# Optimization experiments

Measured on AMD Instinct MI355X. Metric: run time of the kernel, lower is better.

## Reference

```python
import jax, jax.numpy as jnp
import numpy as np
import math

B, S, H, Dh, Dr, HID, C = 2, 2048, 16, 128, 64, 2048, 512

def _linear(x, w, b):
    return x @ w.T + b

def _rope(x):
    # x: [B, H, S, Dr]; interleaved-pair rotation as in the torch module
    d = x.shape[-1]
    s = x.shape[2]
    inv_freq = 1.0 / (10000.0 ** (jnp.arange(0, d, 2, dtype=jnp.float32) / d))
    sinusoid = jnp.arange(s, dtype=jnp.float32)[:, None] * inv_freq[None, :]  # [S, d/2]
    sin, cos = jnp.sin(sinusoid), jnp.cos(sinusoid)  # broadcast over B,H
    x1 = x[..., 0::2]
    x2 = x[..., 1::2]
    rot = jnp.stack([x1 * cos - x2 * sin, x1 * sin + x2 * cos], axis=-1)
    return rot.reshape(x.shape)

def setup_inputs() -> dict:
    key = jax.random.key(0)
    ks = jax.random.split(key, 9)
    sc = 0.02
    return {
        "x": jax.random.normal(ks[0], (B, S, HID), jnp.float32),
        "d_kv_w": jax.random.normal(ks[1], (C, HID), jnp.float32) * sc,
        "d_kv_b": jnp.zeros((C,), jnp.float32),
        "u_k_w": jax.random.normal(ks[2], (H * Dh, C), jnp.float32) * sc,
        "u_k_b": jnp.zeros((H * Dh,), jnp.float32),
        "u_v_w": jax.random.normal(ks[3], (H * Dh, C), jnp.float32) * sc,
        "u_v_b": jnp.zeros((H * Dh,), jnp.float32),
        "d_q_w": jax.random.normal(ks[4], (C, HID), jnp.float32) * sc,
        "d_q_b": jnp.zeros((C,), jnp.float32),
        "u_q_w": jax.random.normal(ks[5], (H * Dh, C), jnp.float32) * sc,
        "u_q_b": jnp.zeros((H * Dh,), jnp.float32),
        "qr_w": jax.random.normal(ks[6], (H * Dr, C), jnp.float32) * sc,
        "qr_b": jnp.zeros((H * Dr,), jnp.float32),
        "out_w": jax.random.normal(ks[7], (HID, H * Dh), jnp.float32) * sc,
        "out_b": jnp.zeros((HID,), jnp.float32),
    }

def reference(x, d_kv_w, d_kv_b, u_k_w, u_k_b, u_v_w, u_v_b,
              d_q_w, d_q_b, u_q_w, u_q_b, qr_w, qr_b, out_w, out_b):
    b, s, _ = x.shape
    kv_c = _linear(x, d_kv_w, d_kv_b)                      # [B,S,C]
    k_c = _linear(kv_c, u_k_w, u_k_b).reshape(b, s, H, Dh)
    k_r = _linear(kv_c, qr_w, qr_b).reshape(b, s, H, Dr)   # note: qr_proj reused, as in source
    v = _linear(kv_c, u_v_w, u_v_b).reshape(b, s, H, Dh)
    q_c_lat = _linear(x, d_q_w, d_q_b)                     # [B,S,C]
    q_c = _linear(q_c_lat, u_q_w, u_q_b).reshape(b, s, H, Dh)
    q_r = _linear(q_c_lat, qr_w, qr_b).reshape(b, s, H, Dr)
    # RoPE operates on [B,H,S,Dr]
    q_r = _rope(q_r.transpose(0, 2, 1, 3)).transpose(0, 2, 1, 3)
    k_r = _rope(k_r.transpose(0, 2, 1, 3)).transpose(0, 2, 1, 3)
    q = jnp.concatenate([q_c, q_r], axis=-1)               # [B,S,H,Dh+Dr]
    k = jnp.concatenate([k_c, k_r], axis=-1)
    scale = 1.0 / math.sqrt(Dh + Dr)
    scores = jnp.einsum('bqhd,bkhd->bhqk', q, k) * scale   # [B,H,S,S]
    probs = jax.nn.softmax(scores, axis=-1)
    ctx = jnp.einsum('bhqk,bkhd->bqhd', probs, v).reshape(b, s, H * Dh)
    return _linear(ctx, out_w, out_b)
```

## Files before the change

kernel.cpp:

```cpp
#include <hip/hip_runtime.h>
#include <hip/hip_bf16.h>
#include <math.h>
#include <stdint.h>

#define NB 2
#define NS 2048
#define NH 16
#define NDH 128
#define NDR 64
#define NHID 2048
#define NC 512

typedef unsigned short u16;
typedef short short8 __attribute__((ext_vector_type(8)));
typedef short short4v __attribute__((ext_vector_type(4)));
typedef float f32x4 __attribute__((ext_vector_type(4)));
typedef float f32x16 __attribute__((ext_vector_type(16)));
typedef int int2v __attribute__((ext_vector_type(2)));

#define SC2 0.10411757f

template <int V> struct IC { static constexpr int value = V; };

__device__ __forceinline__ u16 f2bf(float f) {
  union { float f; uint32_t u; } c; c.f = f;
  uint32_t u = c.u + 0x7fffu + ((c.u >> 16) & 1u);
  return (u16)(u >> 16);
}
__device__ __forceinline__ void async16(const void* g, void* l) {
  __builtin_amdgcn_global_load_lds((const __attribute__((address_space(1))) void*)g,
                                   (__attribute__((address_space(3))) void*)l, 16, 0, 0);
}
__device__ __forceinline__ int cvtpk(float a, float b) {
  int r;
  asm("v_cvt_pk_bf16_f32 %0, %1, %2" : "=v"(r) : "v"(a), "v"(b));
  return r;
}
__device__ __forceinline__ void fsincos(float ang, float& sn, float& cs) {
  float rev = ang * 0.15915494309189535f;
  rev = rev - floorf(rev);
  float s, c;
  asm("v_sin_f32 %0, %1" : "=v"(s) : "v"(rev));
  asm("v_cos_f32 %0, %1" : "=v"(c) : "v"(rev));
  sn = s; cs = c;
}

struct CastArgs {
  const float* src[8];
  u16* dst[8];
  int start[8];
};

__global__ __launch_bounds__(256) void cast_kernel(CastArgs a) {
  int blk = blockIdx.x;
  int ti = 0;
#pragma unroll
  for (int i = 1; i < 8; ++i) ti += (blk >= a.start[i]) ? 1 : 0;
  size_t off = (size_t)(blk - a.start[ti]) * 2048 + (size_t)threadIdx.x * 8;
  const float4* s = (const float4*)(a.src[ti] + off);
  float4 v0 = s[0], v1 = s[1];
  u16 o[8];
  o[0] = f2bf(v0.x); o[1] = f2bf(v0.y); o[2] = f2bf(v0.z); o[3] = f2bf(v0.w);
  o[4] = f2bf(v1.x); o[5] = f2bf(v1.y); o[6] = f2bf(v1.z); o[7] = f2bf(v1.w);
  *(short8*)(a.dst[ti] + off) = *(short8*)o;
}

struct GemmSeg {
  const u16* A;
  const u16* W;
  const float* bias;
  void* dst;
  int K;
  int mode;
  int ldc;
  float oscale;
};
struct GemmArgs {
  GemmSeg seg[5];
  int nbstart[6];
  int nseg;
};

template <int BN>
__global__ __launch_bounds__(512) void gemm_bt(GemmArgs ga) {
  constexpr int NJ = BN / 64;
  constexpr int BUF = 8192 + BN * 64;
  __shared__ char glds[2 * BUF];
  const int nb = blockIdx.x, mb = blockIdx.y;
  int si = 0;
  for (int i = 1; i < ga.nseg; ++i) si += (nb >= ga.nbstart[i]) ? 1 : 0;
  GemmSeg sg = ga.seg[si];
  const int nbl = nb - ga.nbstart[si];
  const int K = sg.K;
  const int t = threadIdx.x;
  const int l = t & 63, w = t >> 6;
  const int r0 = t >> 2, c0 = (t & 3) * 8;
  const int wm = (w >> 2) * 64;
  const int wn = (w & 3) * (BN / 4);
  const int frow = l & 15, fk = (l >> 4) * 8;
  const int lafO = ((wm + frow) * 32 + fk) * 2;
  const int lbfO = 8192 + ((wn + frow) * 32 + fk) * 2;

  const u16* apA = sg.A + (size_t)mb * 128 * K + (size_t)r0 * K + c0;
  const u16* wpA = sg.W + (size_t)nbl * BN * K + (size_t)r0 * K + c0;

  auto stage = [&](int bufOff) {
    async16(apA, glds + bufOff + t * 16);
    async16(wpA, glds + bufOff + 8192 + t * 16);
    if constexpr (BN == 256)
      async16(wpA + (size_t)128 * K, glds + bufOff + 16384 + t * 16);
    apA += 32; wpA += 32;
  };

  const f32x4 vzero = {0.f, 0.f, 0.f, 0.f};
  f32x4 acc[4][NJ];
#pragma unroll
  for (int i = 0; i < 4; ++i)
#pragma unroll
    for (int j = 0; j < NJ; ++j) acc[i][j] = vzero;

  stage(0);
  const int nk = K / 32;

  auto ktile = [&](auto bufc, bool stageNext) {
    constexpr int BO = decltype(bufc)::value;
    if (stageNext) {
      stage(BO ^ BUF);
      if constexpr (BN == 256)
        asm volatile("s_waitcnt vmcnt(3)" ::: "memory");
      else
        asm volatile("s_waitcnt vmcnt(2)" ::: "memory");
    } else {
      asm volatile("s_waitcnt vmcnt(0)" ::: "memory");
    }
    __builtin_amdgcn_s_barrier();
    asm volatile("" ::: "memory");
    short8 af[4], bfr[NJ];
#pragma unroll
    for (int i = 0; i < 4; ++i) af[i] = *(const short8*)(glds + BO + lafO + i * 1024);
#pragma unroll
    for (int j = 0; j < NJ; ++j) bfr[j] = *(const short8*)(glds + BO + lbfO + j * 1024);
    __builtin_amdgcn_s_setprio(1);
#pragma unroll
    for (int i = 0; i < 4; ++i)
#pragma unroll
      for (int j = 0; j < NJ; ++j)
        acc[i][j] = __builtin_amdgcn_mfma_f32_16x16x32_bf16(af[i], bfr[j], acc[i][j], 0, 0, 0);
    __builtin_amdgcn_s_setprio(0);
    asm volatile("s_waitcnt lgkmcnt(0)" ::: "memory");
    __builtin_amdgcn_s_barrier();
  };

  for (int kk = 0; kk < nk; kk += 2) {
    ktile(IC<0>{}, true);
    ktile(IC<BUF>{}, kk + 2 < nk);
  }

  const int rb = (l >> 4) * 4;
  const int cl = l & 15;
  const int mode = sg.mode;
  if (mode == 0) {
    u16* D = (u16*)sg.dst;
    float os = sg.oscale;
#pragma unroll
    for (int i = 0; i < 4; ++i)
#pragma unroll
      for (int j = 0; j < NJ; ++j) {
        int col = nbl * BN + wn + j * 16 + cl;
        float bv = sg.bias[col];
#pragma unroll
        for (int r = 0; r < 4; ++r) {
          int row = mb * 128 + wm + i * 16 + rb + r;
          D[(size_t)row * sg.ldc + col] = f2bf((acc[i][j][r] + bv) * os);
        }
      }
  } else if (mode == 2) {
    float* D = (float*)sg.dst;
#pragma unroll
    for (int i = 0; i < 4; ++i)
#pragma unroll
      for (int j = 0; j < NJ; ++j) {
        int col = nbl * BN + wn + j * 16 + cl;
        float bv = sg.bias[col];
#pragma unroll
        for (int r = 0; r < 4; ++r) {
          int row = mb * 128 + wm + i * 16 + rb + r;
          D[(size_t)row * sg.ldc + col] = acc[i][j][r] + bv;
        }
      }
  } else if (mode == 1) {
    u16* D = (u16*)sg.dst;
#pragma unroll
    for (int i = 0; i < 4; ++i) {
      int row0 = mb * 128 + wm + i * 16 + rb;
      int bb = row0 >> 11, s = row0 & (NS - 1);
#pragma unroll
      for (int j = 0; j < NJ; ++j) {
        int col = nbl * BN + wn + j * 16 + cl;
        int hh = col >> 7, dv = col & 127;
        float bv = sg.bias[col];
        u16 pk[4];
#pragma unroll
        for (int r = 0; r < 4; ++r) pk[r] = f2bf(acc[i][j][r] + bv);
        size_t cell = ((size_t)((bb * NH + hh) * (NS / 8) + (s >> 3)) * 128 + dv) * 8 + (s & 7);
        *(short4v*)(D + cell) = *(short4v*)pk;
      }
    }
  } else if (mode == 4) {
    u16* D = (u16*)sg.dst;
#pragma unroll
    for (int i = 0; i < 4; ++i) {
      int row0 = mb * 128 + wm + i * 16 + rb;
      int bb = row0 >> 11, s = row0 & (NS - 1);
#pragma unroll
      for (int j = 0; j < NJ; ++j) {
        int col = nbl * BN + wn + j * 16 + cl;
        int hh = col >> 7, d = col & 127;
        float bv = sg.bias[col];
        size_t base = ((size_t)((bb * NH + hh) * 24 + (d >> 3)) * NS + s) * 8 + (d & 7);
#pragma unroll
        for (int r = 0; r < 4; ++r) D[base + r * 8] = f2bf(acc[i][j][r] + bv);
      }
    }
  } else if (mode == 5) {
    u16* D = (u16*)sg.dst;
#pragma unroll
    for (int i = 0; i < 4; ++i) {
      int row0 = mb * 128 + wm + i * 16 + rb;
      int bb = row0 >> 11, s = row0 & (NS - 1);
#pragma unroll
      for (int j = 0; j < NJ; ++j) {
        int col = nbl * BN + wn + j * 16 + cl;
        int hh = col >> 6, dr = col & 63;
        int jp = dr >> 1;
        bool ev = !(dr & 1);
        float invf = exp2f(-(float)jp * 0.41524101186f);
        float bv = sg.bias[col];
        size_t base = ((size_t)((bb * NH + hh) * 24 + 16 + (dr >> 3)) * NS + s) * 8 + (dr & 7);
#pragma unroll
        for (int r = 0; r < 4; ++r) {
          float v = acc[i][j][r] + bv;
          float p = __shfl_xor(v, 1);
          float sn, cs;
          fsincos((float)(s + r) * invf, sn, cs);
          float out = ev ? (v * cs - p * sn) : (p * sn + v * cs);
          D[base + r * 8] = f2bf(out);
        }
      }
    }
  } else {
    u16* D = (u16*)sg.dst;
    float os = sg.oscale;
#pragma unroll
    for (int i = 0; i < 4; ++i) {
      int row0 = mb * 128 + wm + i * 16 + rb;
      int s = row0 & (NS - 1);
#pragma unroll
      for (int j = 0; j < NJ; ++j) {
        int col = nbl * BN + wn + j * 16 + cl;
        int dr = col & 63;
        int jp = dr >> 1;
        bool ev = !(dr & 1);
        float invf = exp2f(-(float)jp * 0.41524101186f);
        float bv = sg.bias[col];
#pragma unroll
        for (int r = 0; r < 4; ++r) {
          float v = acc[i][j][r] + bv;
          float p = __shfl_xor(v, 1);
          float sn, cs;
          fsincos((float)(s + r) * invf, sn, cs);
          float out = ev ? (v * cs - p * sn) : (p * sn + v * cs);
          D[(size_t)(row0 + r) * sg.ldc + col] = f2bf(out * os);
        }
      }
    }
  }
}

__global__ __launch_bounds__(256, 2) void attn_kernel(
    const u16* __restrict__ Qc, const u16* __restrict__ Qr,
    const u16* __restrict__ Ktb, const u16* __restrict__ Vtb,
    u16* __restrict__ Ctx) {
  extern __shared__ char smem[];
  const int t = threadIdx.x, w = t >> 6, l = t & 63;
  const int hi = l >> 5, q32 = l & 31;
  const int lin = blockIdx.x;
  const int xcd = lin & 7, idx = lin >> 3;
  const int bh = xcd * 4 + (idx >> 4);
  const int qb = idx & 15;
  const int b = bh >> 4, h = bh & 15;
  const int q0 = qb * 128 + w * 32;

  short8 qf[12];
  {
    const u16* qcp = Qc + ((size_t)(b * NS + q0 + q32)) * NHID + h * NDH + hi * 8;
    const u16* qrp = Qr + ((size_t)(b * NS + q0 + q32)) * (NH * NDR) + h * NDR + hi * 8;
#pragma unroll
    for (int dw = 0; dw < 8; ++dw) qf[dw] = *(const short8*)(qcp + dw * 16);
#pragma unroll
    for (int dw = 0; dw < 4; ++dw) qf[8 + dw] = *(const short8*)(qrp + dw * 16);
  }
#pragma unroll
  for (int dw = 0; dw < 12; ++dw) asm volatile("" :: "v"(qf[dw]));

  const int w2 = t >> 6;
  const u16* kp[6];
#pragma unroll
  for (int r = 0; r < 6; ++r)
    kp[r] = Ktb + ((size_t)(bh * 24 + r * 4 + w2) * NS + l) * 8;
  const u16* vp = Vtb + (size_t)bh * NS * 128 + t * 8;

  const int kbase = q32 * 16 + hi * 1024;
  const int vbase = 24576 + q32 * 16 + hi * 2048;

  f32x16 acc[4], accS, fz;
#pragma unroll
  for (int r = 0; r < 16; ++r) { fz[r] = 0.f; accS[r] = 0.f; }
#pragma unroll
  for (int i = 0; i < 4; ++i) acc[i] = fz;
  union { int i[4]; short8 s; } ONES;
  ONES.i[0] = 0x3F803F80; ONES.i[1] = 0x3F803F80;
  ONES.i[2] = 0x3F803F80; ONES.i[3] = 0x3F803F80;

  auto stage_into = [&](int bufOff) {
#pragma unroll
    for (int r = 0; r < 6; ++r) { async16(kp[r], smem + bufOff + r * 4096 + t * 16); kp[r] += 512; }
#pragma unroll
    for (int r = 0; r < 4; ++r) async16(vp + r * 2048, smem + bufOff + 24576 + r * 4096 + t * 16);
    vp += 8192;
  };
  stage_into(0);

  auto pv_block = [&](const f32x16& s, int n, const char* vb) {
#pragma unroll
    for (int w2i = 0; w2i < 2; ++w2i) {
      const int bse = w2i * 8;
      float p0 = exp2f(s[bse + 0]), p1 = exp2f(s[bse + 1]);
      float p2 = exp2f(s[bse + 2]), p3 = exp2f(s[bse + 3]);
      float p4 = exp2f(s[bse + 4]), p5 = exp2f(s[bse + 5]);
      float p6 = exp2f(s[bse + 6]), p7 = exp2f(s[bse + 7]);
      int A0 = cvtpk(p0, p1);
      int A1 = cvtpk(p2, p3);
      int B0 = cvtpk(p4, p5);
      int B1 = cvtpk(p6, p7);
      int2v r02 = __builtin_amdgcn_permlane32_swap(A0, B0, false, false);
      int2v r13 = __builtin_amdgcn_permlane32_swap(A1, B1, false, false);
      union { int i[4]; short8 s; } F;
      F.i[0] = r02[0]; F.i[1] = r13[0]; F.i[2] = r02[1]; F.i[3] = r13[1];
      const int W = n * 2 + w2i;
      __builtin_amdgcn_s_setprio(1);
#pragma unroll
      for (int d32 = 0; d32 < 4; ++d32) {
        short8 va = *(const short8*)(vb + W * 4096 + d32 * 512);
        acc[d32] = __builtin_amdgcn_mfma_f32_32x32x16_bf16(va, F.s, acc[d32], 0, 0, 0);
      }
      accS = __builtin_amdgcn_mfma_f32_32x32x16_bf16(ONES.s, F.s, accS, 0, 0, 0);
      __builtin_amdgcn_s_setprio(0);
    }
  };

  auto tile = [&](auto bufc, bool stageNext) {
    constexpr int BO = decltype(bufc)::value;
    if (stageNext) {
      stage_into(BO ^ 40960);
      asm volatile("s_waitcnt vmcnt(10)" ::: "memory");
    } else {
      asm volatile("s_waitcnt vmcnt(0)" ::: "memory");
    }
    __builtin_amdgcn_s_barrier();
    asm volatile("" ::: "memory");

    f32x16 sa0, sa1;
    {
      short8 k0 = *(const short8*)(smem + BO + kbase);
      short8 k1 = *(const short8*)(smem + BO + kbase + 512);
      __builtin_amdgcn_s_setprio(1);
      sa0 = __builtin_amdgcn_mfma_f32_32x32x16_bf16(k0, qf[0], fz, 0, 0, 0);
      sa1 = __builtin_amdgcn_mfma_f32_32x32x16_bf16(k1, qf[0], fz, 0, 0, 0);
      __builtin_amdgcn_s_setprio(0);
    }
#pragma unroll
    for (int dw = 1; dw < 12; ++dw) {
      short8 k0 = *(const short8*)(smem + BO + kbase + dw * 2048);
      short8 k1 = *(const short8*)(smem + BO + kbase + dw * 2048 + 512);
      __builtin_amdgcn_s_setprio(1);
      sa0 = __builtin_amdgcn_mfma_f32_32x32x16_bf16(k0, qf[dw], sa0, 0, 0, 0);
      sa1 = __builtin_amdgcn_mfma_f32_32x32x16_bf16(k1, qf[dw], sa1, 0, 0, 0);
      __builtin_amdgcn_s_setprio(0);
    }

    const char* vb = (const char*)smem + BO + vbase;
    pv_block(sa0, 0, vb);
    pv_block(sa1, 1, vb);

    asm volatile("s_waitcnt lgkmcnt(0)" ::: "memory");
    __builtin_amdgcn_s_barrier();
  };

  for (int kv = 0; kv < NS / 64; kv += 2) {
    tile(IC<0>{}, true);
    tile(IC<40960>{}, kv + 2 < NS / 64);
  }

  float invq = 1.f / accS[0];
  u16* dst = Ctx + ((size_t)(b * NS + q0 + q32)) * NHID + h * NDH + hi * 4;
#pragma unroll
  for (int d32 = 0; d32 < 4; ++d32)
#pragma unroll
    for (int m2x = 0; m2x < 4; ++m2x) {
      float a0 = acc[d32][m2x * 4 + 0] * invq, a1 = acc[d32][m2x * 4 + 1] * invq;
      float a2 = acc[d32][m2x * 4 + 2] * invq, a3 = acc[d32][m2x * 4 + 3] * invq;
      union { int i[2]; short4v s; } pu;
      pu.i[0] = cvtpk(a0, a1);
      pu.i[1] = cvtpk(a2, a3);
      *(short4v*)(dst + d32 * 32 + m2x * 8) = pu.s;
    }
}

extern "C" void kernel_launch(void* const* d_in, const int* in_sizes, int n_in,
                              void* d_out, int out_size, void* d_ws, size_t ws_size,
                              hipStream_t stream) {
  (void)in_sizes; (void)n_in; (void)out_size;
  const float* x      = (const float*)d_in[0];
  const float* d_kv_w = (const float*)d_in[1];
  const float* d_kv_b = (const float*)d_in[2];
  const float* u_k_w  = (const float*)d_in[3];
  const float* u_k_b  = (const float*)d_in[4];
  const float* u_v_w  = (const float*)d_in[5];
  const float* u_v_b  = (const float*)d_in[6];
  const float* d_q_w  = (const float*)d_in[7];
  const float* d_q_b  = (const float*)d_in[8];
  const float* u_q_w  = (const float*)d_in[9];
  const float* u_q_b  = (const float*)d_in[10];
  const float* qr_w   = (const float*)d_in[11];
  const float* qr_b   = (const float*)d_in[12];
  const float* out_w  = (const float*)d_in[13];
  const float* out_b  = (const float*)d_in[14];

  char* ws = (char*)d_ws;
  size_t off = 0;
  auto alloc = [&](size_t bytes) -> void* {
    void* p = ws + off;
    off += (bytes + 255) & ~(size_t)255;
    return p;
  };
  u16* xb   = (u16*)alloc((size_t)NB * NS * NHID * 2);
  u16* wdkv = (u16*)alloc((size_t)NC * NHID * 2);
  u16* wuk  = (u16*)alloc((size_t)NH * NDH * NC * 2);
  u16* wuv  = (u16*)alloc((size_t)NH * NDH * NC * 2);
  u16* wdq  = (u16*)alloc((size_t)NC * NHID * 2);
  u16* wuq  = (u16*)alloc((size_t)NH * NDH * NC * 2);
  u16* wqr  = (u16*)alloc((size_t)NH * NDR * NC * 2);
  u16* wout = (u16*)alloc((size_t)NHID * NH * NDH * 2);
  u16* kvc  = (u16*)alloc((size_t)NB * NS * NC * 2);
  u16* qlat = (u16*)alloc((size_t)NB * NS * NC * 2);
  u16* Ktb  = (u16*)alloc((size_t)NB * NH * 24 * NS * 8 * 2);
  u16* Vtb  = (u16*)alloc((size_t)NB * NH * NS * NDH * 2);
  u16* Qc   = (u16*)alloc((size_t)NB * NS * NH * NDH * 2);
  u16* Qrt  = (u16*)alloc((size_t)NB * NS * NH * NDR * 2);
  u16* ctx  = xb;
  if (off > ws_size) return;

  {
    CastArgs ca;
    const float* srcs[8] = {x, d_kv_w, u_k_w, u_v_w, d_q_w, u_q_w, qr_w, out_w};
    u16* dsts[8] = {xb, wdkv, wuk, wuv, wdq, wuq, wqr, wout};
    int sizes[8] = {NB * NS * NHID, NC * NHID, NH * NDH * NC, NH * NDH * NC,
                    NC * NHID, NH * NDH * NC, NH * NDR * NC, NHID * NH * NDH};
    int st = 0;
    for (int i = 0; i < 8; ++i) {
      ca.src[i] = srcs[i]; ca.dst[i] = dsts[i]; ca.start[i] = st;
      st += sizes[i] / 2048;
    }
    cast_kernel<<<dim3(st), dim3(256), 0, stream>>>(ca);
  }

  {
    GemmArgs ga;
    ga.nseg = 2;
    ga.seg[0] = {xb, wdkv, d_kv_b, kvc, NHID, 0, NC, 1.f};
    ga.seg[1] = {xb, wdq,  d_q_b,  qlat, NHID, 0, NC, 1.f};
    for (int i = 2; i < 5; ++i) ga.seg[i] = ga.seg[0];
    ga.nbstart[0] = 0; ga.nbstart[1] = 4; ga.nbstart[2] = 8;
    ga.nbstart[3] = 8; ga.nbstart[4] = 8; ga.nbstart[5] = 8;
    gemm_bt<128><<<dim3(8, 32), dim3(512), 0, stream>>>(ga);
  }

  {
    GemmArgs ga;
    ga.nseg = 5;
    ga.seg[0] = {kvc,  wuk, u_k_b, Ktb, NC, 4, 0, 1.f};
    ga.seg[1] = {kvc,  wuv, u_v_b, Vtb, NC, 1, 0, 1.f};
    ga.seg[2] = {kvc,  wqr, qr_b,  Ktb, NC, 5, 0, 1.f};
    ga.seg[3] = {qlat, wuq, u_q_b, Qc,  NC, 0, NH * NDH, SC2};
    ga.seg[4] = {qlat, wqr, qr_b,  Qrt, NC, 3, NH * NDR, SC2};
    ga.nbstart[0] = 0;  ga.nbstart[1] = 8;  ga.nbstart[2] = 16;
    ga.nbstart[3] = 20; ga.nbstart[4] = 28; ga.nbstart[5] = 32;
    gemm_bt<256><<<dim3(32, 32), dim3(512), 0, stream>>>(ga);
  }

  hipFuncSetAttribute((const void*)attn_kernel,
                      hipFuncAttributeMaxDynamicSharedMemorySize, 81920);
  attn_kernel<<<dim3(512), dim3(256), 81920, stream>>>(Qc, Qrt, Ktb, Vtb, ctx);

  {
    GemmArgs ga;
    ga.nseg = 1;
    ga.seg[0] = {ctx, wout, out_b, d_out, NHID, 2, NHID, 1.f};
    for (int i = 1; i < 5; ++i) ga.seg[i] = ga.seg[0];
    ga.nbstart[0] = 0;
    for (int i = 1; i < 6; ++i) ga.nbstart[i] = 8;
    gemm_bt<256><<<dim3(8, 32), dim3(512), 0, stream>>>(ga);
  }
}
```

Before: 254.8 us.

## Replace double-buffered K/V staging with single buffer in attention kernel

The attention kernel drops its two-buffer async prefetch of K/V tiles and uses a single 40KB LDS buffer. Each iteration waits for all loads, computes, then issues the next tile's loads after the trailing barrier. This halves LDS use, which may let more blocks share a CU, but it serialises global loads with compute so load latency is no longer hidden.

```diff
diff --git a/kernel.cpp b/kernel.cpp
--- a/kernel.cpp
+++ b/kernel.cpp
@@ -322,14 +322,14 @@
   ONES.i[0] = 0x3F803F80; ONES.i[1] = 0x3F803F80;
   ONES.i[2] = 0x3F803F80; ONES.i[3] = 0x3F803F80;
 
-  auto stage_into = [&](int bufOff) {
-#pragma unroll
-    for (int r = 0; r < 6; ++r) { async16(kp[r], smem + bufOff + r * 4096 + t * 16); kp[r] += 512; }
-#pragma unroll
-    for (int r = 0; r < 4; ++r) async16(vp + r * 2048, smem + bufOff + 24576 + r * 4096 + t * 16);
+  auto stage_into = [&]() {
+#pragma unroll
+    for (int r = 0; r < 6; ++r) { async16(kp[r], smem + r * 4096 + t * 16); kp[r] += 512; }
+#pragma unroll
+    for (int r = 0; r < 4; ++r) async16(vp + r * 2048, smem + 24576 + r * 4096 + t * 16);
     vp += 8192;
   };
-  stage_into(0);
+  stage_into();
 
   auto pv_block = [&](const f32x16& s, int n, const char* vb) {
 #pragma unroll
@@ -359,21 +359,15 @@
     }
   };
 
-  auto tile = [&](auto bufc, bool stageNext) {
-    constexpr int BO = decltype(bufc)::value;
-    if (stageNext) {
-      stage_into(BO ^ 40960);
-      asm volatile("s_waitcnt vmcnt(10)" ::: "memory");
-    } else {
-      asm volatile("s_waitcnt vmcnt(0)" ::: "memory");
-    }
+  for (int kv = 0; kv < NS / 64; ++kv) {
+    asm volatile("s_waitcnt vmcnt(0)" ::: "memory");
     __builtin_amdgcn_s_barrier();
     asm volatile("" ::: "memory");
 
     f32x16 sa0, sa1;
     {
-      short8 k0 = *(const short8*)(smem + BO + kbase);
-      short8 k1 = *(const short8*)(smem + BO + kbase + 512);
+      short8 k0 = *(const short8*)(smem + kbase);
+      short8 k1 = *(const short8*)(smem + kbase + 512);
       __builtin_amdgcn_s_setprio(1);
       sa0 = __builtin_amdgcn_mfma_f32_32x32x16_bf16(k0, qf[0], fz, 0, 0, 0);
       sa1 = __builtin_amdgcn_mfma_f32_32x32x16_bf16(k1, qf[0], fz, 0, 0, 0);
@@ -381,25 +375,21 @@
     }
 #pragma unroll
     for (int dw = 1; dw < 12; ++dw) {
-      short8 k0 = *(const short8*)(smem + BO + kbase + dw * 2048);
-      short8 k1 = *(const short8*)(smem + BO + kbase + dw * 2048 + 512);
+      short8 k0 = *(const short8*)(smem + kbase + dw * 2048);
+      short8 k1 = *(const short8*)(smem + kbase + dw * 2048 + 512);
       __builtin_amdgcn_s_setprio(1);
       sa0 = __builtin_amdgcn_mfma_f32_32x32x16_bf16(k0, qf[dw], sa0, 0, 0, 0);
       sa1 = __builtin_amdgcn_mfma_f32_32x32x16_bf16(k1, qf[dw], sa1, 0, 0, 0);
       __builtin_amdgcn_s_setprio(0);
     }
 
-    const char* vb = (const char*)smem + BO + vbase;
+    const char* vb = (const char*)smem + vbase;
     pv_block(sa0, 0, vb);
     pv_block(sa1, 1, vb);
 
     asm volatile("s_waitcnt lgkmcnt(0)" ::: "memory");
     __builtin_amdgcn_s_barrier();
-  };
-
-  for (int kv = 0; kv < NS / 64; kv += 2) {
-    tile(IC<0>{}, true);
-    tile(IC<40960>{}, kv + 2 < NS / 64);
+    if (kv + 1 < NS / 64) stage_into();
   }
 
   float invq = 1.f / accS[0];
@@ -500,8 +490,8 @@
   }
 
   hipFuncSetAttribute((const void*)attn_kernel,
-                      hipFuncAttributeMaxDynamicSharedMemorySize, 81920);
-  attn_kernel<<<dim3(512), dim3(256), 81920, stream>>>(Qc, Qrt, Ktb, Vtb, ctx);
+                      hipFuncAttributeMaxDynamicSharedMemorySize, 40960);
+  attn_kernel<<<dim3(512), dim3(256), 40960, stream>>>(Qc, Qrt, Ktb, Vtb, ctx);
 
   {
     GemmArgs ga;
```

After: 256.4 us. About the same (+0.6%).
